# Optimization experiments

Measured on AMD Instinct MI355X. Metric: run time of the kernel, lower is better.

## Reference

```python
import jax, jax.numpy as jnp
import numpy as np

B, L, D, N, F, V, NL, NS = 2, 1024, 768, 16, 3072, 32000, 4, 3
EPS = 1e-5


def _layernorm(x, g, b):
    m = x.mean(-1, keepdims=True)
    v = ((x - m) ** 2).mean(-1, keepdims=True)
    return (x - m) / jnp.sqrt(v + EPS) * g + b


def _ssm_sublayer(x, cw, A_log, WB, WC, Wdt, dtb, Dsk):
    # x: [B,L,D]; causal depthwise conv, kernel_size=3
    xp = jnp.pad(x, ((0, 0), (2, 0), (0, 0)))
    u = xp[:, :-2] * cw[:, 0] + xp[:, 1:-1] * cw[:, 1] + xp[:, 2:] * cw[:, 2]
    u = jax.nn.silu(u)
    dt = jax.nn.softplus(jnp.einsum('bld,de->ble', u, Wdt) + dtb)   # [B,L,D]
    Bm = jnp.einsum('bld,dn->bln', u, WB)                           # [B,L,N]
    Cm = jnp.einsum('bld,dn->bln', u, WC)                           # [B,L,N]
    A = -jnp.exp(A_log)                                             # [D,N]

    def step(h, t):
        dt_t, u_t, b_t, c_t = t                                     # [B,D],[B,D],[B,N],[B,N]
        h = jnp.exp(dt_t[..., None] * A) * h + (dt_t * u_t)[..., None] * b_t[:, None, :]
        y = jnp.einsum('bdn,bn->bd', h, c_t)
        return h, y

    h0 = jnp.zeros((x.shape[0], x.shape[2], A.shape[1]), x.dtype)
    _, ys = jax.lax.scan(step, h0, (dt.transpose(1, 0, 2), u.transpose(1, 0, 2),
                                    Bm.transpose(1, 0, 2), Cm.transpose(1, 0, 2)))
    return ys.transpose(1, 0, 2) + Dsk * u


def setup_inputs() -> dict:
    key = jax.random.key(0)
    ks = jax.random.split(key, 16)
    g = lambda k, shape, s=0.02: jax.random.normal(k, shape, jnp.float32) * s
    inp = {
        'x': jax.random.randint(ks[0], (B, L), 0, V),
        'emb': g(ks[1], (V, D)),
        'conv_w': g(ks[2], (NL, NS, D, 3), 0.2),
        'A_log': jnp.log(jnp.tile(jnp.arange(1, N + 1, dtype=jnp.float32), (NL, NS, D, 1))),
        'W_B': g(ks[3], (NL, NS, D, N)),
        'W_C': g(ks[4], (NL, NS, D, N)),
        'W_dt': g(ks[5], (NL, NS, D, D)),
        'dt_bias': jnp.full((NL, NS, D), -4.0, jnp.float32),
        'D_skip': jnp.ones((NL, NS, D), jnp.float32),
        'ffn_W1': g(ks[6], (NL, D, F)),
        'ffn_b1': jnp.zeros((NL, F), jnp.float32),
        'ffn_W2': g(ks[7], (NL, F, D)),
        'ffn_b2': jnp.zeros((NL, D), jnp.float32),
        'norm_g': jnp.ones((D,), jnp.float32),
        'norm_b': jnp.zeros((D,), jnp.float32),
        'out_W': g(ks[8], (D, V)),
        'out_b': jnp.zeros((V,), jnp.float32),
    }
    return inp


def reference(x, emb, conv_w, A_log, W_B, W_C, W_dt, dt_bias, D_skip,
              ffn_W1, ffn_b1, ffn_W2, ffn_b2, norm_g, norm_b, out_W, out_b):
    h = emb[x]                                                      # [B,L,D]
    for l in range(NL):
        for s in range(NS):
            h = h + _ssm_sublayer(h, conv_w[l, s], A_log[l, s], W_B[l, s],
                                  W_C[l, s], W_dt[l, s], dt_bias[l, s], D_skip[l, s])
        f = jax.nn.gelu(jnp.einsum('bld,df->blf', h, ffn_W1[l]) + ffn_b1[l], approximate=False)
        h = h + jnp.einsum('blf,fd->bld', f, ffn_W2[l]) + ffn_b2[l]
    h = _layernorm(h, norm_g, norm_b)
    logits = jnp.einsum('bld,dv->blv', h, out_W) + out_b            # [B,L,V]
    return logits
```

## Files before the change

kernel.cpp:

```cpp
#include <hip/hip_runtime.h>
#include <hip/hip_bf16.h>
#include <math.h>

#define BB 2
#define LL 1024
#define DD 768
#define NN 16
#define FF 3072
#define VV 32000
#define NLL 4
#define NSS 3
#define BL (BB*LL)
#define CHK 64
#define CLEN (LL/CHK)

typedef __bf16 bf16x8 __attribute__((ext_vector_type(8)));
typedef float f32x4 __attribute__((ext_vector_type(4)));
typedef short short8 __attribute__((ext_vector_type(8)));

typedef __attribute__((address_space(1))) const void gconst_t;
typedef __attribute__((address_space(3))) void lds_t;

__device__ __forceinline__ void g2l16(const void* g, void* l) {
  __builtin_amdgcn_global_load_lds((gconst_t*)g, (lds_t*)l, 16, 0, 0);
}



__global__ __launch_bounds__(256) void k_embed(
    const int* __restrict__ x, const float* __restrict__ emb,
    float* __restrict__ h) {
  int row = blockIdx.x;
  int idx = x[row];
  const float* e = emb + (size_t)idx * DD;
  float* hr = h + (size_t)row * DD;
  int t = threadIdx.x;
  hr[t]       = e[t];
  hr[t + 256] = e[t + 256];
  hr[t + 512] = e[t + 512];
}

__global__ __launch_bounds__(256) void k_conv(
    const float* __restrict__ h, const float* __restrict__ cw,
    __hip_bfloat16* __restrict__ ub) {
  int row = blockIdx.x;
  int l = row & (LL - 1);
  #pragma unroll
  for (int d = threadIdx.x; d < DD; d += 256) {
    float w0 = cw[d * 3 + 0], w1 = cw[d * 3 + 1], w2 = cw[d * 3 + 2];
    float v = h[(size_t)row * DD + d] * w2;
    if (l >= 1) v += h[(size_t)(row - 1) * DD + d] * w1;
    if (l >= 2) v += h[(size_t)(row - 2) * DD + d] * w0;
    float sv = v / (1.f + __expf(-v));
    ub[(size_t)row * DD + d] = __float2bfloat16(sv);
  }
}

__global__ __launch_bounds__(256) void k_layernorm(
    const float* __restrict__ x, const float* __restrict__ g,
    const float* __restrict__ bta, __hip_bfloat16* __restrict__ o) {
  int row = blockIdx.x;
  const float* xr = x + (size_t)row * DD;
  int tid = threadIdx.x;
  float v1 = xr[tid], v2 = xr[tid + 256], v3 = xr[tid + 512];
  float s = v1 + v2 + v3;
  float sq = v1 * v1 + v2 * v2 + v3 * v3;
  #pragma unroll
  for (int m = 1; m < 64; m <<= 1) {
    s  += __shfl_xor(s, m);
    sq += __shfl_xor(sq, m);
  }
  __shared__ float ss[4], sqs[4];
  if ((tid & 63) == 0) { ss[tid >> 6] = s; sqs[tid >> 6] = sq; }
  __syncthreads();
  s  = ss[0] + ss[1] + ss[2] + ss[3];
  sq = sqs[0] + sqs[1] + sqs[2] + sqs[3];
  float mean = s * (1.f / DD);
  float var  = sq * (1.f / DD) - mean * mean;
  float rstd = rsqrtf(var + 1e-5f);
  o[(size_t)row * DD + tid]       = __float2bfloat16((v1 - mean) * rstd * g[tid]       + bta[tid]);
  o[(size_t)row * DD + tid + 256] = __float2bfloat16((v2 - mean) * rstd * g[tid + 256] + bta[tid + 256]);
  o[(size_t)row * DD + tid + 512] = __float2bfloat16((v3 - mean) * rstd * g[tid + 512] + bta[tid + 512]);
}

#define S1 1728
#define S2 1740
#define S3 4044
#define S4 6348
#define SEND 12348

__global__ __launch_bounds__(256) void k_wconv_all(
    const float* __restrict__ Wdt, const float* __restrict__ WB,
    const float* __restrict__ WC, const float* __restrict__ W1,
    const float* __restrict__ W2, const float* __restrict__ Wout,
    __hip_bfloat16* __restrict__ WTdt, __hip_bfloat16* __restrict__ WT1,
    __hip_bfloat16* __restrict__ WT2, __hip_bfloat16* __restrict__ WTlog) {
  __shared__ float T[64][65];
  int bid = blockIdx.x;
  int tid = threadIdx.x;

  if (bid >= S1 && bid < S2) {
    int sub = bid - S1;
    const float* WBp = WB + (size_t)sub * DD * NN;
    const float* WCp = WC + (size_t)sub * DD * NN;
    __hip_bfloat16* dst = WTdt + (size_t)sub * 832 * DD;
    for (int e = tid; e < 64 * DD; e += 256) {
      int r = e / DD, k = e - (e / DD) * DD;
      float v = 0.f;
      if (r < 16)      v = WBp[(size_t)k * NN + r];
      else if (r < 32) v = WCp[(size_t)k * NN + (r - 16)];
      dst[(size_t)(768 + r) * DD + k] = __float2bfloat16(v);
    }
    return;
  }

  const float* W; __hip_bfloat16* WT;
  int K, N, n0, k0;
  if (bid < S1) {
    int sub = bid / 144, t = bid % 144;
    W = Wdt + (size_t)sub * DD * DD; WT = WTdt + (size_t)sub * 832 * DD;
    K = DD; N = DD; n0 = (t % 12) * 64; k0 = (t / 12) * 64;
  } else if (bid < S3) {
    int idx = bid - S2, l = idx / 576, t = idx % 576;
    W = W1 + (size_t)l * DD * FF; WT = WT1 + (size_t)l * FF * DD;
    K = DD; N = FF; n0 = (t % 48) * 64; k0 = (t / 48) * 64;
  } else if (bid < S4) {
    int idx = bid - S3, l = idx / 576, t = idx % 576;
    W = W2 + (size_t)l * FF * DD; WT = WT2 + (size_t)l * DD * FF;
    K = FF; N = DD; n0 = (t % 12) * 64; k0 = (t / 12) * 64;
  } else {
    int t = bid - S4;
    W = Wout; WT = WTlog;
    K = DD; N = VV; n0 = (t % 500) * 64; k0 = (t / 500) * 64;
  }

  int c = tid & 63, r4 = tid >> 6;
  #pragma unroll
  for (int i = 0; i < 16; ++i) {
    int k_l = r4 + i * 4;
    T[k_l][c] = W[(size_t)(k0 + k_l) * N + n0 + c];
  }
  __syncthreads();
  #pragma unroll
  for (int i = 0; i < 16; ++i) {
    int n_l = r4 + i * 4;
    WT[(size_t)(n0 + n_l) * K + k0 + c] = __float2bfloat16(T[c][n_l]);
  }
}

__device__ __forceinline__ float softplus_f(float x) {
  return (x > 20.f) ? x : log1pf(__expf(x));
}
__device__ __forceinline__ float gelu_f(float x) {
  return 0.5f * x * (1.f + erff(x * 0.70710678118654752f));
}

__global__ __launch_bounds__(256) void k_gemm_ffn1(
    const __hip_bfloat16* __restrict__ A, const __hip_bfloat16* __restrict__ BT,
    const float* __restrict__ bias, __hip_bfloat16* __restrict__ Cb) {
  __shared__ __align__(16) __hip_bfloat16 As[128 * 64];
  __shared__ __align__(16) __hip_bfloat16 Bs[128 * 64];
  const int tid = threadIdx.x;
  const int lane = tid & 63, wid = tid >> 6;
  int wg = (blockIdx.x & 7) * 48 + (blockIdx.x >> 3);
  int tn = wg % 24, tm = wg / 24;
  const int bm = tm * 128, bn = tn * 128;
  const int wm = wid >> 1, wn = wid & 1;
  const int sr = lane >> 3;
  const int sks = (((lane & 7) ^ (lane >> 3)) & 7) * 8;
  const int N = FF, K = DD;

  f32x4 acc[4][4] = {};

  for (int k0 = 0; k0 < K; k0 += 64) {
    __syncthreads();
    #pragma unroll
    for (int cc = 0; cc < 4; ++cc) {
      int ch = wid * 4 + cc;
      int row = ch * 8 + sr;
      g2l16(A  + (size_t)(bm + row) * K + k0 + sks, &As[ch * 512]);
      g2l16(BT + (size_t)(bn + row) * K + k0 + sks, &Bs[ch * 512]);
    }
    __syncthreads();
    #pragma unroll
    for (int kk = 0; kk < 2; ++kk) {
      int koff = (((kk * 4 + (lane >> 4)) ^ (lane & 7)) & 7) * 8;
      bf16x8 af[4], bfr[4];
      #pragma unroll
      for (int m = 0; m < 4; ++m)
        af[m] = *(const bf16x8*)&As[(wm * 64 + m * 16 + (lane & 15)) * 64 + koff];
      #pragma unroll
      for (int n = 0; n < 4; ++n)
        bfr[n] = *(const bf16x8*)&Bs[(wn * 64 + n * 16 + (lane & 15)) * 64 + koff];
      #pragma unroll
      for (int m = 0; m < 4; ++m)
        #pragma unroll
        for (int n = 0; n < 4; ++n)
          acc[m][n] = __builtin_amdgcn_mfma_f32_16x16x32_bf16(af[m], bfr[n], acc[m][n], 0, 0, 0);
    }
  }

  const int crow0 = (lane >> 4) * 4;
  const int ccol = lane & 15;
  #pragma unroll
  for (int m = 0; m < 4; ++m) {
    #pragma unroll
    for (int n = 0; n < 4; ++n) {
      int col = bn + wn * 64 + n * 16 + ccol;
      float bv = bias[col];
      #pragma unroll
      for (int j = 0; j < 4; ++j) {
        int row = bm + wm * 64 + m * 16 + crow0 + j;
        Cb[(size_t)row * N + col] = __float2bfloat16(gelu_f(acc[m][n][j] + bv));
      }
    }
  }
}

__global__ __launch_bounds__(256) void k_gemm_dtbc64(
    const __hip_bfloat16* __restrict__ A, const __hip_bfloat16* __restrict__ BT,
    const float* __restrict__ dtbias, __hip_bfloat16* __restrict__ dtbb,
    float* __restrict__ Bm, float* __restrict__ Cm) {
  __shared__ __align__(16) __hip_bfloat16 As[64 * 64];
  __shared__ __align__(16) __hip_bfloat16 Bs[64 * 64];
  const int tid = threadIdx.x;
  const int lane = tid & 63, wid = tid >> 6;
  int wg = (blockIdx.x & 7) * 52 + (blockIdx.x >> 3);
  int tn = wg % 13, tm = wg / 13;
  const int bm = tm * 64, bn = tn * 64;
  const int wm = wid >> 1, wn = wid & 1;
  const int sr = lane >> 3;
  const int sks = (((lane & 7) ^ (lane >> 3)) & 7) * 8;

  f32x4 acc[2][2] = {};

  for (int k0 = 0; k0 < DD; k0 += 64) {
    __syncthreads();
    #pragma unroll
    for (int cc = 0; cc < 2; ++cc) {
      int ch = wid * 2 + cc;
      int row = ch * 8 + sr;
      g2l16(A  + (size_t)(bm + row) * DD + k0 + sks, &As[ch * 512]);
      g2l16(BT + (size_t)(bn + row) * DD + k0 + sks, &Bs[ch * 512]);
    }
    __syncthreads();
    #pragma unroll
    for (int kk = 0; kk < 2; ++kk) {
      int koff = (((kk * 4 + (lane >> 4)) ^ (lane & 7)) & 7) * 8;
      bf16x8 af[2], bfr[2];
      #pragma unroll
      for (int m = 0; m < 2; ++m)
        af[m] = *(const bf16x8*)&As[(wm * 32 + m * 16 + (lane & 15)) * 64 + koff];
      #pragma unroll
      for (int n = 0; n < 2; ++n)
        bfr[n] = *(const bf16x8*)&Bs[(wn * 32 + n * 16 + (lane & 15)) * 64 + koff];
      #pragma unroll
      for (int m = 0; m < 2; ++m)
        #pragma unroll
        for (int n = 0; n < 2; ++n)
          acc[m][n] = __builtin_amdgcn_mfma_f32_16x16x32_bf16(af[m], bfr[n], acc[m][n], 0, 0, 0);
    }
  }

  const int crow0 = (lane >> 4) * 4;
  const int ccol = lane & 15;
  #pragma unroll
  for (int m = 0; m < 2; ++m) {
    #pragma unroll
    for (int n = 0; n < 2; ++n) {
      int col = bn + wn * 32 + n * 16 + ccol;
      if (col >= 800) continue;
      float bv = (col < DD) ? dtbias[col] : 0.f;
      #pragma unroll
      for (int j = 0; j < 4; ++j) {
        int row = bm + wm * 32 + m * 16 + crow0 + j;
        float v = acc[m][n][j] + bv;
        if (col < DD)       dtbb[(size_t)row * DD + col] = __float2bfloat16(softplus_f(v));
        else if (col < 784) Bm[(size_t)row * NN + (col - DD)] = v;
        else                Cm[(size_t)row * NN + (col - 784)] = v;
      }
    }
  }
}

__global__ __launch_bounds__(256) void k_gemm_ffn2s(
    const __hip_bfloat16* __restrict__ A, const __hip_bfloat16* __restrict__ BT,
    const float* __restrict__ bias, float* __restrict__ h) {
  __shared__ __align__(16) __hip_bfloat16 As[64 * 64];
  __shared__ __align__(16) __hip_bfloat16 Bs[64 * 64];
  const int tid = threadIdx.x;
  const int lane = tid & 63, wid = tid >> 6;
  int wg = (blockIdx.x & 7) * 96 + (blockIdx.x >> 3);
  int tile = wg % 384, split = wg / 384;
  int tm = tile % 32, tn = tile / 32;
  const int bm = tm * 64, bn = tn * 64;
  const int wm = wid >> 1, wn = wid & 1;
  const int sr = lane >> 3;
  const int sks = (((lane & 7) ^ (lane >> 3)) & 7) * 8;
  const int kbeg = split * (FF / 2), kend = kbeg + FF / 2;

  f32x4 acc[2][2] = {};

  for (int k0 = kbeg; k0 < kend; k0 += 64) {
    __syncthreads();
    #pragma unroll
    for (int cc = 0; cc < 2; ++cc) {
      int ch = wid * 2 + cc;
      int row = ch * 8 + sr;
      g2l16(A  + (size_t)(bm + row) * FF + k0 + sks, &As[ch * 512]);
      g2l16(BT + (size_t)(bn + row) * FF + k0 + sks, &Bs[ch * 512]);
    }
    __syncthreads();
    #pragma unroll
    for (int kk = 0; kk < 2; ++kk) {
      int koff = (((kk * 4 + (lane >> 4)) ^ (lane & 7)) & 7) * 8;
      bf16x8 af[2], bfr[2];
      #pragma unroll
      for (int m = 0; m < 2; ++m)
        af[m] = *(const bf16x8*)&As[(wm * 32 + m * 16 + (lane & 15)) * 64 + koff];
      #pragma unroll
      for (int n = 0; n < 2; ++n)
        bfr[n] = *(const bf16x8*)&Bs[(wn * 32 + n * 16 + (lane & 15)) * 64 + koff];
      #pragma unroll
      for (int m = 0; m < 2; ++m)
        #pragma unroll
        for (int n = 0; n < 2; ++n)
          acc[m][n] = __builtin_amdgcn_mfma_f32_16x16x32_bf16(af[m], bfr[n], acc[m][n], 0, 0, 0);
    }
  }

  const int crow0 = (lane >> 4) * 4;
  const int ccol = lane & 15;
  #pragma unroll
  for (int m = 0; m < 2; ++m) {
    #pragma unroll
    for (int n = 0; n < 2; ++n) {
      int col = bn + wn * 32 + n * 16 + ccol;
      float bv = (split == 0) ? bias[col] : 0.f;
      #pragma unroll
      for (int j = 0; j < 4; ++j) {
        int row = bm + wm * 32 + m * 16 + crow0 + j;
        unsafeAtomicAdd(&h[(size_t)row * DD + col], acc[m][n][j] + bv);
      }
    }
  }
}

__global__ __launch_bounds__(512) void k_gemm_logits2(
    const __hip_bfloat16* __restrict__ A, const __hip_bfloat16* __restrict__ BT,
    const float* __restrict__ bias, float* __restrict__ C, int M, int N, int K) {
  __shared__ __align__(16) __hip_bfloat16 As[256 * 64];
  __shared__ __align__(16) __hip_bfloat16 Bs[128 * 64];
  const int tid = threadIdx.x;
  const int lane = tid & 63, wid = tid >> 6;
  int bid = blockIdx.y * gridDim.x + blockIdx.x;
  int mt = bid & 7, nt = bid >> 3;
  const int bm = mt * 256, bn = nt * 128;
  const int wm = wid >> 1, wn = wid & 1;
  const int sr = lane >> 3;
  const int sks = (((lane & 7) ^ (lane >> 3)) & 7) * 8;

  f32x4 acc[4][4] = {};

  for (int k0 = 0; k0 < K; k0 += 64) {
    __syncthreads();
    #pragma unroll
    for (int r = 0; r < 4; ++r) {
      int ch = r * 8 + wid;
      int row = ch * 8 + sr;
      g2l16(A + (size_t)(bm + row) * K + k0 + sks, &As[ch * 512]);
    }
    #pragma unroll
    for (int r = 0; r < 2; ++r) {
      int ch = r * 8 + wid;
      int row = ch * 8 + sr;
      g2l16(BT + (size_t)(bn + row) * K + k0 + sks, &Bs[ch * 512]);
    }
    __syncthreads();
    #pragma unroll
    for (int kk = 0; kk < 2; ++kk) {
      int koff = (((kk * 4 + (lane >> 4)) ^ (lane & 7)) & 7) * 8;
      bf16x8 af[4], bfr[4];
      #pragma unroll
      for (int m = 0; m < 4; ++m)
        af[m] = *(const bf16x8*)&As[(wm * 64 + m * 16 + (lane & 15)) * 64 + koff];
      #pragma unroll
      for (int n = 0; n < 4; ++n)
        bfr[n] = *(const bf16x8*)&Bs[(wn * 64 + n * 16 + (lane & 15)) * 64 + koff];
      #pragma unroll
      for (int m = 0; m < 4; ++m)
        #pragma unroll
        for (int n = 0; n < 4; ++n)
          acc[m][n] = __builtin_amdgcn_mfma_f32_16x16x32_bf16(af[m], bfr[n], acc[m][n], 0, 0, 0);
    }
  }

  const int crow0 = (lane >> 4) * 4;
  const int ccol = lane & 15;
  #pragma unroll
  for (int m = 0; m < 4; ++m) {
    #pragma unroll
    for (int n = 0; n < 4; ++n) {
      int col = bn + wn * 64 + n * 16 + ccol;
      float bv = bias[col];
      #pragma unroll
      for (int j = 0; j < 4; ++j) {
        int row = bm + wm * 64 + m * 16 + crow0 + j;
        C[(size_t)row * N + col] = acc[m][n][j] + bv;
      }
    }
  }
}

__global__ __launch_bounds__(256) void k_scan_a(
    const __hip_bfloat16* __restrict__ dt, const __hip_bfloat16* __restrict__ ub,
    const float* __restrict__ Bm, const float* __restrict__ A_log,
    __hip_bfloat16* __restrict__ F, float* __restrict__ SD) {
  int c = blockIdx.x;
  int bd = blockIdx.y;
  int b = bd / 3;
  int d = (bd % 3) * 256 + threadIdx.x;
  float Av[16];
  {
    const float4* al = (const float4*)(A_log + (size_t)d * NN);
    #pragma unroll
    for (int q = 0; q < 4; ++q) {
      float4 v = al[q];
      Av[q * 4 + 0] = -__expf(v.x);
      Av[q * 4 + 1] = -__expf(v.y);
      Av[q * 4 + 2] = -__expf(v.z);
      Av[q * 4 + 3] = -__expf(v.w);
    }
  }
  float h[16];
  #pragma unroll
  for (int n = 0; n < 16; ++n) h[n] = 0.f;
  float sdt = 0.f;
  size_t base = ((size_t)b * LL + (size_t)c * CLEN) * DD + d;
  int row0 = c * CLEN + b * LL;
  #pragma unroll 4
  for (int t = 0; t < CLEN; ++t) {
    float dtv = __bfloat162float(dt[base + (size_t)t * DD]);
    float uv  = __bfloat162float(ub[base + (size_t)t * DD]);
    float Bv[16];
    const float4* bp = (const float4*)(Bm + (size_t)(row0 + t) * NN);
    *(float4*)&Bv[0]  = bp[0];
    *(float4*)&Bv[4]  = bp[1];
    *(float4*)&Bv[8]  = bp[2];
    *(float4*)&Bv[12] = bp[3];
    float du = dtv * uv;
    sdt += dtv;
    #pragma unroll
    for (int n = 0; n < 16; ++n)
      h[n] = __expf(dtv * Av[n]) * h[n] + du * Bv[n];
  }
  alignas(16) __hip_bfloat16 fx[16];
  #pragma unroll
  for (int n = 0; n < 16; ++n) fx[n] = __float2bfloat16(h[n]);
  __hip_bfloat16* fo = F + (((size_t)c * BB + b) * DD + d) * NN;
  *(short8*)&fo[0] = *(short8*)&fx[0];
  *(short8*)&fo[8] = *(short8*)&fx[8];
  SD[((size_t)c * BB + b) * DD + d] = sdt;
}

__global__ __launch_bounds__(256) void k_scan_b(
    const __hip_bfloat16* __restrict__ F, const float* __restrict__ SD,
    const float* __restrict__ A_log, __hip_bfloat16* __restrict__ Hinit) {
  __shared__ float Ls[64 * 17];
  __shared__ float Ho[64 * 17];
  __shared__ float Ss[64];
  int bd = blockIdx.x;
  int b = bd / DD, d = bd % DD;
  int tid = threadIdx.x;
  if (tid < 128) {
    int c = tid >> 1, q = tid & 1;
    alignas(16) __hip_bfloat16 fx[8];
    *(short8*)fx = *(const short8*)(F + (((size_t)c * BB + b) * DD + d) * NN + q * 8);
    #pragma unroll
    for (int i = 0; i < 8; ++i)
      Ls[c * 17 + q * 8 + i] = __bfloat162float(fx[i]);
  }
  if (tid < 64) Ss[tid] = SD[((size_t)tid * BB + b) * DD + d];
  __syncthreads();
  int lane = tid & 63, w = tid >> 6;
  #pragma unroll
  for (int r = 0; r < 4; ++r) {
    int n = w * 4 + r;
    float Av = -__expf(A_log[(size_t)d * NN + n]);
    float Fv = Ls[lane * 17 + n];
    float Dv = __expf(Ss[lane] * Av);
    #pragma unroll
    for (int s = 1; s < 64; s <<= 1) {
      float Fp = __shfl_up(Fv, s);
      float Dp = __shfl_up(Dv, s);
      float nF = Fv + Dv * Fp;
      float nD = Dv * Dp;
      Fv = (lane >= s) ? nF : Fv;
      Dv = (lane >= s) ? nD : Dv;
    }
    float Hi = __shfl_up(Fv, 1);
    if (lane == 0) Hi = 0.f;
    Ho[lane * 17 + n] = Hi;
  }
  __syncthreads();
  if (tid < 128) {
    int c = tid >> 1, q = tid & 1;
    alignas(16) __hip_bfloat16 hx[8];
    #pragma unroll
    for (int i = 0; i < 8; ++i)
      hx[i] = __float2bfloat16(Ho[c * 17 + q * 8 + i]);
    *(short8*)(Hinit + (((size_t)c * BB + b) * DD + d) * NN + q * 8) = *(short8*)hx;
  }
}

__global__ __launch_bounds__(256) void k_scan_c(
    const __hip_bfloat16* __restrict__ dt, const __hip_bfloat16* __restrict__ ub,
    const float* __restrict__ Bm, const float* __restrict__ Cm,
    const float* __restrict__ A_log, const float* __restrict__ Dsk,
    const __hip_bfloat16* __restrict__ Hinit, float* __restrict__ hres,
    __hip_bfloat16* __restrict__ hb, int writeHb) {
  int c = blockIdx.x;
  int bd = blockIdx.y;
  int b = bd / 3;
  int d = (bd % 3) * 256 + threadIdx.x;
  float Av[16];
  {
    const float4* al = (const float4*)(A_log + (size_t)d * NN);
    #pragma unroll
    for (int q = 0; q < 4; ++q) {
      float4 v = al[q];
      Av[q * 4 + 0] = -__expf(v.x);
      Av[q * 4 + 1] = -__expf(v.y);
      Av[q * 4 + 2] = -__expf(v.z);
      Av[q * 4 + 3] = -__expf(v.w);
    }
  }
  float h[16];
  {
    alignas(16) __hip_bfloat16 hx[16];
    const __hip_bfloat16* hi = Hinit + (((size_t)c * BB + b) * DD + d) * NN;
    *(short8*)&hx[0] = *(const short8*)&hi[0];
    *(short8*)&hx[8] = *(const short8*)&hi[8];
    #pragma unroll
    for (int n = 0; n < 16; ++n) h[n] = __bfloat162float(hx[n]);
  }
  float dskip = Dsk[d];
  size_t base = ((size_t)b * LL + (size_t)c * CLEN) * DD + d;
  int row0 = c * CLEN + b * LL;
  #pragma unroll 4
  for (int t = 0; t < CLEN; ++t) {
    float dtv = __bfloat162float(dt[base + (size_t)t * DD]);
    float uv  = __bfloat162float(ub[base + (size_t)t * DD]);
    float Bv[16], Cv[16];
    const float4* bp = (const float4*)(Bm + (size_t)(row0 + t) * NN);
    const float4* cp = (const float4*)(Cm + (size_t)(row0 + t) * NN);
    *(float4*)&Bv[0]  = bp[0];
    *(float4*)&Bv[4]  = bp[1];
    *(float4*)&Bv[8]  = bp[2];
    *(float4*)&Bv[12] = bp[3];
    *(float4*)&Cv[0]  = cp[0];
    *(float4*)&Cv[4]  = cp[1];
    *(float4*)&Cv[8]  = cp[2];
    *(float4*)&Cv[12] = cp[3];
    float du = dtv * uv;
    float y = 0.f;
    #pragma unroll
    for (int n = 0; n < 16; ++n) {
      h[n] = __expf(dtv * Av[n]) * h[n] + du * Bv[n];
      y += h[n] * Cv[n];
    }
    float nh = hres[base + (size_t)t * DD] + y + dskip * uv;
    hres[base + (size_t)t * DD] = nh;
    if (writeHb) hb[base + (size_t)t * DD] = __float2bfloat16(nh);
  }
}

extern "C" void kernel_launch(void* const* d_in, const int* in_sizes, int n_in,
                              void* d_out, int out_size, void* d_ws, size_t ws_size,
                              hipStream_t stream) {
  const int*   x     = (const int*)d_in[0];
  const float* emb   = (const float*)d_in[1];
  const float* convw = (const float*)d_in[2];
  const float* A_log = (const float*)d_in[3];
  const float* W_B   = (const float*)d_in[4];
  const float* W_C   = (const float*)d_in[5];
  const float* W_dt  = (const float*)d_in[6];
  const float* dt_b  = (const float*)d_in[7];
  const float* D_sk  = (const float*)d_in[8];
  const float* W1    = (const float*)d_in[9];
  const float* b1    = (const float*)d_in[10];
  const float* W2    = (const float*)d_in[11];
  const float* b2    = (const float*)d_in[12];
  const float* ng    = (const float*)d_in[13];
  const float* nb    = (const float*)d_in[14];
  const float* Wout  = (const float*)d_in[15];
  const float* bout  = (const float*)d_in[16];
  float* out = (float*)d_out;

  __hip_bfloat16* WTdt = (__hip_bfloat16*)d_out;
  __hip_bfloat16* WT1  = WTdt + (size_t)12 * 832 * DD;
  __hip_bfloat16* WT2  = WT1  + (size_t)NLL * FF * DD;

  char* p = (char*)d_ws;
  auto alloc = [&](size_t bytes) { char* r = p; p += (bytes + 255) & ~(size_t)255; return r; };
  float* h    = (float*)alloc((size_t)BL * DD * 4);
  float* Bm   = (float*)alloc((size_t)BL * NN * 4);
  float* Cm   = (float*)alloc((size_t)BL * NN * 4);
  float* SD   = (float*)alloc((size_t)CHK * BB * DD * 4);
  __hip_bfloat16* dtbb  = (__hip_bfloat16*)alloc((size_t)BL * DD * 2);
  __hip_bfloat16* F     = (__hip_bfloat16*)alloc((size_t)CHK * BB * DD * NN * 2);
  __hip_bfloat16* Hini  = (__hip_bfloat16*)alloc((size_t)CHK * BB * DD * NN * 2);
  __hip_bfloat16* ub    = (__hip_bfloat16*)alloc((size_t)BL * DD * 2);
  __hip_bfloat16* hb    = (__hip_bfloat16*)alloc((size_t)BL * DD * 2);
  __hip_bfloat16* fb    = (__hip_bfloat16*)alloc((size_t)BL * FF * 2);
  __hip_bfloat16* lnb   = (__hip_bfloat16*)alloc((size_t)BL * DD * 2);
  __hip_bfloat16* WTlog = (__hip_bfloat16*)alloc((size_t)VV * DD * 2);

  k_wconv_all<<<SEND, 256, 0, stream>>>(
      W_dt, W_B, W_C, W1, W2, Wout, WTdt, WT1, WT2, WTlog);
  k_embed<<<BL, 256, 0, stream>>>(x, emb, h);

  for (int l = 0; l < NLL; ++l) {
    for (int s = 0; s < NSS; ++s) {
      int ls = l * NSS + s;
      k_conv<<<BL, 256, 0, stream>>>(h, convw + (size_t)ls * DD * 3, ub);
      k_gemm_dtbc64<<<416, 256, 0, stream>>>(
          ub, WTdt + (size_t)ls * 832 * DD, dt_b + (size_t)ls * DD, dtbb, Bm, Cm);
      k_scan_a<<<dim3(CHK, 6), 256, 0, stream>>>(
          dtbb, ub, Bm, A_log + (size_t)ls * DD * NN, F, SD);
      k_scan_b<<<BB * DD, 256, 0, stream>>>(
          F, SD, A_log + (size_t)ls * DD * NN, Hini);
      k_scan_c<<<dim3(CHK, 6), 256, 0, stream>>>(
          dtbb, ub, Bm, Cm, A_log + (size_t)ls * DD * NN, D_sk + (size_t)ls * DD,
          Hini, h, hb, (s == NSS - 1) ? 1 : 0);
    }
    k_gemm_ffn1<<<384, 256, 0, stream>>>(
        hb, WT1 + (size_t)l * FF * DD, b1 + (size_t)l * FF, fb);
    k_gemm_ffn2s<<<768, 256, 0, stream>>>(
        fb, WT2 + (size_t)l * DD * FF, b2 + (size_t)l * DD, h);
  }

  k_layernorm<<<BL, 256, 0, stream>>>(h, ng, nb, lnb);
  k_gemm_logits2<<<dim3(VV / 128, BL / 256), 512, 0, stream>>>(
      lnb, WTlog, bout, out, BL, VV, DD);
}
```

Measured before the change: 1.138 ms.

## Fold inter-chunk scan into scan_c and stage logits epilogue through LDS

Removes the separate k_scan_b kernel and its Hinit buffer. Each k_scan_c block now rebuilds its initial state by walking all earlier chunk summaries sequentially, which saves a launch and a round trip through global memory. The cost is redundant quadratic work, since late chunks read up to 63 summaries. Separately, the logits GEMM epilogue is staged through shared memory so it can write coalesced float4 rows instead of scattered scalar stores.

```diff
diff --git a/kernel.cpp b/kernel.cpp
--- a/kernel.cpp
+++ b/kernel.cpp
@@ -349,8 +349,9 @@
 __global__ __launch_bounds__(512) void k_gemm_logits2(
     const __hip_bfloat16* __restrict__ A, const __hip_bfloat16* __restrict__ BT,
     const float* __restrict__ bias, float* __restrict__ C, int M, int N, int K) {
-  __shared__ __align__(16) __hip_bfloat16 As[256 * 64];
-  __shared__ __align__(16) __hip_bfloat16 Bs[128 * 64];
+  __shared__ __align__(16) char smem[(256 * 64 + 128 * 64) * 2];
+  __hip_bfloat16* As = (__hip_bfloat16*)smem;
+  __hip_bfloat16* Bs = (__hip_bfloat16*)(smem + 256 * 64 * 2);
   const int tid = threadIdx.x;
   const int lane = tid & 63, wid = tid >> 6;
   int bid = blockIdx.y * gridDim.x + blockIdx.x;
@@ -395,18 +396,29 @@
     }
   }
 
+  __syncthreads();
+  float* eps = (float*)smem + (size_t)wid * 1088;
   const int crow0 = (lane >> 4) * 4;
   const int ccol = lane & 15;
+  const int gcolbase = bn + wn * 64;
   #pragma unroll
   for (int m = 0; m < 4; ++m) {
     #pragma unroll
     for (int n = 0; n < 4; ++n) {
-      int col = bn + wn * 64 + n * 16 + ccol;
-      float bv = bias[col];
-      #pragma unroll
-      for (int j = 0; j < 4; ++j) {
-        int row = bm + wm * 64 + m * 16 + crow0 + j;
-        C[(size_t)row * N + col] = acc[m][n][j] + bv;
+      float bv = bias[gcolbase + n * 16 + ccol];
+      #pragma unroll
+      for (int j = 0; j < 4; ++j)
+        eps[(crow0 + j) * 68 + n * 16 + ccol] = acc[m][n][j] + bv;
+    }
+    int growbase = bm + wm * 64 + m * 16;
+    #pragma unroll
+    for (int p = 0; p < 2; ++p) {
+      int r = (lane >> 3) + 8 * p;
+      #pragma unroll
+      for (int i = 0; i < 2; ++i) {
+        int s4 = (lane & 7) + 8 * i;
+        float4 v = *(float4*)&eps[r * 68 + s4 * 4];
+        *(float4*)&C[(size_t)(growbase + r) * N + gcolbase + s4 * 4] = v;
       }
     }
   }
@@ -463,62 +475,12 @@
   SD[((size_t)c * BB + b) * DD + d] = sdt;
 }
 
-__global__ __launch_bounds__(256) void k_scan_b(
-    const __hip_bfloat16* __restrict__ F, const float* __restrict__ SD,
-    const float* __restrict__ A_log, __hip_bfloat16* __restrict__ Hinit) {
-  __shared__ float Ls[64 * 17];
-  __shared__ float Ho[64 * 17];
-  __shared__ float Ss[64];
-  int bd = blockIdx.x;
-  int b = bd / DD, d = bd % DD;
-  int tid = threadIdx.x;
-  if (tid < 128) {
-    int c = tid >> 1, q = tid & 1;
-    alignas(16) __hip_bfloat16 fx[8];
-    *(short8*)fx = *(const short8*)(F + (((size_t)c * BB + b) * DD + d) * NN + q * 8);
-    #pragma unroll
-    for (int i = 0; i < 8; ++i)
-      Ls[c * 17 + q * 8 + i] = __bfloat162float(fx[i]);
-  }
-  if (tid < 64) Ss[tid] = SD[((size_t)tid * BB + b) * DD + d];
-  __syncthreads();
-  int lane = tid & 63, w = tid >> 6;
-  #pragma unroll
-  for (int r = 0; r < 4; ++r) {
-    int n = w * 4 + r;
-    float Av = -__expf(A_log[(size_t)d * NN + n]);
-    float Fv = Ls[lane * 17 + n];
-    float Dv = __expf(Ss[lane] * Av);
-    #pragma unroll
-    for (int s = 1; s < 64; s <<= 1) {
-      float Fp = __shfl_up(Fv, s);
-      float Dp = __shfl_up(Dv, s);
-      float nF = Fv + Dv * Fp;
-      float nD = Dv * Dp;
-      Fv = (lane >= s) ? nF : Fv;
-      Dv = (lane >= s) ? nD : Dv;
-    }
-    float Hi = __shfl_up(Fv, 1);
-    if (lane == 0) Hi = 0.f;
-    Ho[lane * 17 + n] = Hi;
-  }
-  __syncthreads();
-  if (tid < 128) {
-    int c = tid >> 1, q = tid & 1;
-    alignas(16) __hip_bfloat16 hx[8];
-    #pragma unroll
-    for (int i = 0; i < 8; ++i)
-      hx[i] = __float2bfloat16(Ho[c * 17 + q * 8 + i]);
-    *(short8*)(Hinit + (((size_t)c * BB + b) * DD + d) * NN + q * 8) = *(short8*)hx;
-  }
-}
-
 __global__ __launch_bounds__(256) void k_scan_c(
     const __hip_bfloat16* __restrict__ dt, const __hip_bfloat16* __restrict__ ub,
     const float* __restrict__ Bm, const float* __restrict__ Cm,
     const float* __restrict__ A_log, const float* __restrict__ Dsk,
-    const __hip_bfloat16* __restrict__ Hinit, float* __restrict__ hres,
-    __hip_bfloat16* __restrict__ hb, int writeHb) {
+    const __hip_bfloat16* __restrict__ F, const float* __restrict__ SD,
+    float* __restrict__ hres, __hip_bfloat16* __restrict__ hb, int writeHb) {
   int c = blockIdx.x;
   int bd = blockIdx.y;
   int b = bd / 3;
@@ -536,13 +498,17 @@
     }
   }
   float h[16];
-  {
-    alignas(16) __hip_bfloat16 hx[16];
-    const __hip_bfloat16* hi = Hinit + (((size_t)c * BB + b) * DD + d) * NN;
-    *(short8*)&hx[0] = *(const short8*)&hi[0];
-    *(short8*)&hx[8] = *(const short8*)&hi[8];
-    #pragma unroll
-    for (int n = 0; n < 16; ++n) h[n] = __bfloat162float(hx[n]);
+  #pragma unroll
+  for (int n = 0; n < 16; ++n) h[n] = 0.f;
+  for (int cc = 0; cc < c; ++cc) {
+    float sdt = SD[((size_t)cc * BB + b) * DD + d];
+    alignas(16) __hip_bfloat16 fx[16];
+    const __hip_bfloat16* fp = F + (((size_t)cc * BB + b) * DD + d) * NN;
+    *(short8*)&fx[0] = *(const short8*)&fp[0];
+    *(short8*)&fx[8] = *(const short8*)&fp[8];
+    #pragma unroll
+    for (int n = 0; n < 16; ++n)
+      h[n] = __bfloat162float(fx[n]) + __expf(sdt * Av[n]) * h[n];
   }
   float dskip = Dsk[d];
   size_t base = ((size_t)b * LL + (size_t)c * CLEN) * DD + d;
@@ -609,7 +575,6 @@
   float* SD   = (float*)alloc((size_t)CHK * BB * DD * 4);
   __hip_bfloat16* dtbb  = (__hip_bfloat16*)alloc((size_t)BL * DD * 2);
   __hip_bfloat16* F     = (__hip_bfloat16*)alloc((size_t)CHK * BB * DD * NN * 2);
-  __hip_bfloat16* Hini  = (__hip_bfloat16*)alloc((size_t)CHK * BB * DD * NN * 2);
   __hip_bfloat16* ub    = (__hip_bfloat16*)alloc((size_t)BL * DD * 2);
   __hip_bfloat16* hb    = (__hip_bfloat16*)alloc((size_t)BL * DD * 2);
   __hip_bfloat16* fb    = (__hip_bfloat16*)alloc((size_t)BL * FF * 2);
@@ -628,11 +593,9 @@
           ub, WTdt + (size_t)ls * 832 * DD, dt_b + (size_t)ls * DD, dtbb, Bm, Cm);
       k_scan_a<<<dim3(CHK, 6), 256, 0, stream>>>(
           dtbb, ub, Bm, A_log + (size_t)ls * DD * NN, F, SD);
-      k_scan_b<<<BB * DD, 256, 0, stream>>>(
-          F, SD, A_log + (size_t)ls * DD * NN, Hini);
       k_scan_c<<<dim3(CHK, 6), 256, 0, stream>>>(
           dtbb, ub, Bm, Cm, A_log + (size_t)ls * DD * NN, D_sk + (size_t)ls * DD,
-          Hini, h, hb, (s == NSS - 1) ? 1 : 0);
+          F, SD, h, hb, (s == NSS - 1) ? 1 : 0);
     }
     k_gemm_ffn1<<<384, 256, 0, stream>>>(
         hb, WT1 + (size_t)l * FF * DD, b1 + (size_t)l * FF, fb);
```

Result: slower. 1.354 ms (+19.0%).
